# Optimization experiments

Measured on AMD Instinct MI355X. Metric: run time of the kernel, lower is better.

## Reference

```python
import jax, jax.numpy as jnp
import numpy as np

N_NODES = 50000
N_EDGES = 800000
N_GRAPHS = 512
NUM_TYPES = 1000
EMB = 128
HID = 128


def setup_inputs() -> dict:
    key = jax.random.key(0)
    ks = jax.random.split(key, 8)
    x_type = jax.random.randint(ks[0], (N_NODES,), 0, NUM_TYPES, dtype=jnp.int32)
    edge_index = jax.random.randint(ks[1], (2, N_EDGES), 0, N_NODES, dtype=jnp.int32)
    batch = jnp.sort(jax.random.randint(ks[2], (N_NODES,), 0, N_GRAPHS, dtype=jnp.int32))
    emb = jax.random.normal(ks[3], (NUM_TYPES, EMB), jnp.float32)
    s1 = 1.0 / np.sqrt(EMB)
    s2 = 1.0 / np.sqrt(HID)
    W1 = jax.random.normal(ks[4], (EMB, HID), jnp.float32) * s1
    b1 = jnp.zeros((HID,), jnp.float32)
    W2 = jax.random.normal(ks[5], (HID, HID), jnp.float32) * s2
    b2 = jnp.zeros((HID,), jnp.float32)
    return {"x_type": x_type, "edge_index": edge_index, "batch": batch,
            "emb": emb, "W1": W1, "b1": b1, "W2": W2, "b2": b2}


def _gcn_norm(edge_index, n_nodes):
    # PyG GCNConv default: add self-loops, symmetric normalization.
    loops = jnp.arange(n_nodes, dtype=edge_index.dtype)
    src = jnp.concatenate([edge_index[0], loops])  # [E+N]
    dst = jnp.concatenate([edge_index[1], loops])
    deg = jax.ops.segment_sum(jnp.ones_like(dst, jnp.float32), dst, num_segments=n_nodes)
    dis = jax.lax.rsqrt(deg)  # deg >= 1 thanks to self-loops
    norm = dis[src] * dis[dst]  # [E+N]
    return src, dst, norm


def _gcn_conv(x, src, dst, norm, W, b, n_nodes):
    h = x @ W                                  # [N, out]
    msg = h[src] * norm[:, None]               # edge-gathered, normalized messages
    out = jax.ops.segment_sum(msg, dst, num_segments=n_nodes)  # scatter-add
    return out + b


def reference(x_type, edge_index, batch, emb, W1, b1, W2, b2):
    src, dst, norm = _gcn_norm(edge_index, N_NODES)
    x = emb[x_type]                            # [N, EMB]
    x = jax.nn.relu(_gcn_conv(x, src, dst, norm, W1, b1, N_NODES))
    x = _gcn_conv(x, src, dst, norm, W2, b2, N_NODES)
    # index_add_ pooling over graphs (dropout is identity in eval / p=0)
    out = jax.ops.segment_sum(x, batch, num_segments=N_GRAPHS)  # [G, HID]
    return out
```

## Files before the change

### kernel.cpp

```cpp
#include <hip/hip_runtime.h>

#define N_NODES 50000
#define N_EDGES 800000
#define N_GRAPHS 512
#define FDIM 128
#define NTYPES_PAD 1000

#define NBLK 128
#define CHUNK ((N_EDGES + NBLK - 1) / NBLK)
#define NQUAD (N_NODES / 4)
#define NSB ((NQUAD + 127) / 128)
#define NPW 4
#define NW ((N_NODES + NPW - 1) / NPW)

typedef __bf16 bf16x8 __attribute__((ext_vector_type(8)));
typedef float f32x4 __attribute__((ext_vector_type(4)));
union BF8 { bf16x8 v; unsigned short u[8]; };

__device__ __forceinline__ unsigned short f2bf(float f) {
  unsigned int u = __float_as_uint(f);
  unsigned int r = (u + 0x7FFFu + ((u >> 16) & 1u)) >> 16;
  return (unsigned short)r;
}
__device__ __forceinline__ float bflo(unsigned int v) {
  return __uint_as_float(v << 16);
}
__device__ __forceinline__ float bfhi(unsigned int v) {
  return __uint_as_float(v & 0xFFFF0000u);
}

__global__ __launch_bounds__(512) void k_hist(const int* __restrict__ dst,
                                              unsigned int* __restrict__ Hist,
                                              unsigned char* __restrict__ rank8,
                                              int* __restrict__ g_done) {
  __shared__ unsigned int h[NQUAD];
  int b = blockIdx.x, t = threadIdx.x;
  if (b == 0 && t == 0) *g_done = 0;
  for (int i = t; i < NQUAD; i += 512) h[i] = 0;
  __syncthreads();
  int e0 = b * CHUNK, e1 = min(e0 + CHUNK, N_EDGES);
  for (int e = e0 + t; e < e1; e += 512) {
    int d = dst[e];
    unsigned int sh = (d & 3) * 8;
    unsigned int old = atomicAdd(&h[d >> 2], 1u << sh);
    rank8[e] = (unsigned char)((old >> sh) & 0xFFu);
  }
  __syncthreads();
  unsigned int* H = Hist + (size_t)b * NQUAD;
  for (int i = t; i < NQUAD; i += 512) H[i] = h[i];
}

__global__ __launch_bounds__(128) void k_prep(
    const unsigned int* __restrict__ Hist, const int* __restrict__ batch,
    unsigned int* __restrict__ Cur, float* __restrict__ dis,
    int* __restrict__ row_ptr, float* __restrict__ Zb,
    int* __restrict__ gstart, int* __restrict__ g_bsum,
    int* __restrict__ g_done) {
  int blk = blockIdx.x, tid = threadIdx.x;
  int q = blk * 128 + tid;

  for (int i = blk * 128 + tid; i < N_GRAPHS * FDIM; i += NSB * 128)
    Zb[i] = 0.0f;

  if (q < NQUAD) {
    int i0 = 4 * q;
    int prev = (i0 == 0) ? -1 : batch[i0 - 1];
#pragma unroll
    for (int k = 0; k < 4; ++k) {
      int i = i0 + k;
      int bb = batch[i];
      for (int g = prev + 1; g <= bb; ++g) gstart[g] = i;
      prev = bb;
    }
    if (i0 + 3 == N_NODES - 1)
      for (int g = prev + 1; g <= N_GRAPHS; ++g) gstart[g] = N_NODES;
  }

  unsigned int r0 = 0, r1 = 0, r2 = 0, r3 = 0;
  if (q < NQUAD) {
    for (int b = 0; b < NBLK; ++b) {
      unsigned int v = Hist[(size_t)b * NQUAD + q];
      Cur[(size_t)b * NQUAD + q] =
          (r0 & 255u) | ((r1 & 255u) << 8) | ((r2 & 255u) << 16) | (r3 << 24);
      r0 += v & 255u;
      r1 += (v >> 8) & 255u;
      r2 += (v >> 16) & 255u;
      r3 += v >> 24;
    }
    float4 dv = make_float4(rsqrtf((float)r0 + 1.f), rsqrtf((float)r1 + 1.f),
                            rsqrtf((float)r2 + 1.f), rsqrtf((float)r3 + 1.f));
    ((float4*)dis)[q] = dv;
  }

  int tsum = (q < NQUAD) ? (int)(r0 + r1 + r2 + r3) : 0;
  __shared__ int s[128];
  s[tid] = tsum;
  __syncthreads();
  for (int d = 1; d < 128; d <<= 1) {
    int u = (tid >= d) ? s[tid - d] : 0;
    __syncthreads();
    s[tid] += u;
    __syncthreads();
  }
  int excl = s[tid] - tsum;
  int btotal = s[127];

  if (tid == 0) {
    atomicExch(&g_bsum[blk], btotal);
    __threadfence();
    atomicAdd(g_done, 1);
    while (atomicAdd(g_done, 0) < NSB) {
    }
  }
  __syncthreads();
  __shared__ int sb[NSB];
  if (tid < NSB) sb[tid] = atomicAdd(&g_bsum[tid], 0);
  __syncthreads();
  int bpref = 0;
  for (int t = 0; t < blk; ++t) bpref += sb[t];

  if (q < NQUAD) {
    int base = bpref + excl;
    ((int4*)row_ptr)[q] =
        make_int4(base, base + (int)r0, base + (int)(r0 + r1),
                  base + (int)(r0 + r1 + r2));
  }
  if (q == NQUAD - 1) row_ptr[N_NODES] = N_EDGES;
}

__global__ __launch_bounds__(512) void k_fill2(
    const int* __restrict__ src, const int* __restrict__ dst,
    const int* __restrict__ x_type, const int* __restrict__ row_ptr,
    const unsigned int* __restrict__ Cur, const unsigned char* __restrict__ rank8,
    const float* __restrict__ dis, unsigned long long* __restrict__ csr) {
  int e = blockIdx.x * blockDim.x + threadIdx.x;
  if (e >= N_EDGES) return;
  int b = e / CHUNK;
  int s = src[e], d = dst[e];
  unsigned int cw = Cur[(size_t)b * NQUAD + (d >> 2)];
  int base = (int)((cw >> ((d & 3) * 8)) & 0xFFu);
  int pos = row_ptr[d] + base + (int)rank8[e];
  unsigned int lo = (unsigned int)s | ((unsigned int)x_type[s] << 16);
  unsigned int hi = (unsigned int)f2bf(dis[d]);
  csr[pos] = (unsigned long long)lo | ((unsigned long long)hi << 32);
}

__global__ __launch_bounds__(256) void k_embw(
    const float* __restrict__ emb, const float* __restrict__ W1,
    unsigned short* __restrict__ T1) {
  __shared__ unsigned short Ws[128 * 128];
  int t = threadIdx.x, w = t >> 6, l = t & 63;
  for (int i = t; i < 16384; i += 256) {
    int k = i >> 7, n = i & 127;
    Ws[n * 128 + (k ^ ((n & 15) << 3))] = f2bf(W1[i]);
  }
  int row0 = blockIdx.x * 64 + w * 16;
  int arow = row0 + (l & 15);
  bool ok = arow < NTYPES_PAD;
  bf16x8 a[4];
#pragma unroll
  for (int ks = 0; ks < 4; ++ks) {
    BF8 av;
    const float* ap = emb + (size_t)arow * FDIM + (l >> 4) * 8 + ks * 32;
#pragma unroll
    for (int i = 0; i < 8; ++i) av.u[i] = ok ? f2bf(ap[i]) : 0;
    a[ks] = av.v;
  }
  __syncthreads();
  f32x4 acc[8] = {};
#pragma unroll
  for (int ks = 0; ks < 4; ++ks) {
#pragma unroll
    for (int ct = 0; ct < 8; ++ct) {
      int n = ct * 16 + (l & 15);
      int kk = (ks * 32 + (l >> 4) * 8) ^ ((n & 15) << 3);
      bf16x8 b = *(const bf16x8*)&Ws[n * 128 + kk];
      acc[ct] =
          __builtin_amdgcn_mfma_f32_16x16x32_bf16(a[ks], b, acc[ct], 0, 0, 0);
    }
  }
#pragma unroll
  for (int ct = 0; ct < 8; ++ct) {
    int col = ct * 16 + (l & 15);
#pragma unroll
    for (int r = 0; r < 4; ++r) {
      int row = row0 + (l >> 4) * 4 + r;
      if (row < NTYPES_PAD) T1[row * FDIM + col] = f2bf(acc[ct][r]);
    }
  }
}

__global__ void k_agg1(const int* __restrict__ x_type,
                       const unsigned short* __restrict__ T1,
                       const float* __restrict__ b1,
                       const int* __restrict__ row_ptr,
                       const unsigned long long* __restrict__ csr,
                       const float* __restrict__ dis,
                       unsigned int* __restrict__ y1) {
  int gid = blockIdx.x * blockDim.x + threadIdx.x;
  int node = gid >> 6;
  int lane = gid & 63;
  if (node >= N_NODES) return;
  const unsigned int* T = (const unsigned int*)T1;
  const unsigned int* C = (const unsigned int*)csr;
  float di = dis[node];
  unsigned int v = T[(size_t)x_type[node] * 64 + lane];
  float ax = bflo(v) * di, ay = bfhi(v) * di;
  int j = row_ptr[node], end = row_ptr[node + 1];
  for (; j + 8 <= end; j += 8) {
    unsigned int e0 = C[2 * j], e1 = C[2 * j + 2];
    unsigned int e2 = C[2 * j + 4], e3 = C[2 * j + 6];
    unsigned int e4 = C[2 * j + 8], e5 = C[2 * j + 10];
    unsigned int e6 = C[2 * j + 12], e7 = C[2 * j + 14];
    unsigned int u0 = T[(size_t)(e0 >> 16) * 64 + lane];
    unsigned int u1 = T[(size_t)(e1 >> 16) * 64 + lane];
    unsigned int u2 = T[(size_t)(e2 >> 16) * 64 + lane];
    unsigned int u3 = T[(size_t)(e3 >> 16) * 64 + lane];
    unsigned int u4 = T[(size_t)(e4 >> 16) * 64 + lane];
    unsigned int u5 = T[(size_t)(e5 >> 16) * 64 + lane];
    unsigned int u6 = T[(size_t)(e6 >> 16) * 64 + lane];
    unsigned int u7 = T[(size_t)(e7 >> 16) * 64 + lane];
    float n0 = dis[e0 & 0xFFFFu], n1 = dis[e1 & 0xFFFFu];
    float n2 = dis[e2 & 0xFFFFu], n3 = dis[e3 & 0xFFFFu];
    float n4 = dis[e4 & 0xFFFFu], n5 = dis[e5 & 0xFFFFu];
    float n6 = dis[e6 & 0xFFFFu], n7 = dis[e7 & 0xFFFFu];
    ax = fmaf(bflo(u0), n0, ax); ay = fmaf(bfhi(u0), n0, ay);
    ax = fmaf(bflo(u1), n1, ax); ay = fmaf(bfhi(u1), n1, ay);
    ax = fmaf(bflo(u2), n2, ax); ay = fmaf(bfhi(u2), n2, ay);
    ax = fmaf(bflo(u3), n3, ax); ay = fmaf(bfhi(u3), n3, ay);
    ax = fmaf(bflo(u4), n4, ax); ay = fmaf(bfhi(u4), n4, ay);
    ax = fmaf(bflo(u5), n5, ax); ay = fmaf(bfhi(u5), n5, ay);
    ax = fmaf(bflo(u6), n6, ax); ay = fmaf(bfhi(u6), n6, ay);
    ax = fmaf(bflo(u7), n7, ax); ay = fmaf(bfhi(u7), n7, ay);
  }
  for (; j + 4 <= end; j += 4) {
    unsigned int e0 = C[2 * j], e1 = C[2 * j + 2];
    unsigned int e2 = C[2 * j + 4], e3 = C[2 * j + 6];
    unsigned int u0 = T[(size_t)(e0 >> 16) * 64 + lane];
    unsigned int u1 = T[(size_t)(e1 >> 16) * 64 + lane];
    unsigned int u2 = T[(size_t)(e2 >> 16) * 64 + lane];
    unsigned int u3 = T[(size_t)(e3 >> 16) * 64 + lane];
    float n0 = dis[e0 & 0xFFFFu], n1 = dis[e1 & 0xFFFFu];
    float n2 = dis[e2 & 0xFFFFu], n3 = dis[e3 & 0xFFFFu];
    ax = fmaf(bflo(u0), n0, ax); ay = fmaf(bfhi(u0), n0, ay);
    ax = fmaf(bflo(u1), n1, ax); ay = fmaf(bfhi(u1), n1, ay);
    ax = fmaf(bflo(u2), n2, ax); ay = fmaf(bfhi(u2), n2, ay);
    ax = fmaf(bflo(u3), n3, ax); ay = fmaf(bfhi(u3), n3, ay);
  }
  for (; j < end; ++j) {
    unsigned int e = C[2 * j];
    unsigned int u = T[(size_t)(e >> 16) * 64 + lane];
    float nw = dis[e & 0xFFFFu];
    ax = fmaf(bflo(u), nw, ax);
    ay = fmaf(bfhi(u), nw, ay);
  }
  float2 bb = ((const float2*)b1)[lane];
  ax = fmaxf(fmaf(di, ax, bb.x), 0.f) * di;
  ay = fmaxf(fmaf(di, ay, bb.y), 0.f) * di;
  y1[(size_t)node * 64 + lane] = (unsigned int)f2bf(ax) |
                                 ((unsigned int)f2bf(ay) << 16);
}

__global__ void k_aggpool(const unsigned int* __restrict__ y1,
                          const int* __restrict__ row_ptr,
                          const unsigned long long* __restrict__ csr,
                          const float* __restrict__ dis,
                          const int* __restrict__ batch,
                          float* __restrict__ Partials, int* __restrict__ Gid,
                          float* __restrict__ Zb) {
  int gid = blockIdx.x * blockDim.x + threadIdx.x;
  int wid = gid >> 6;
  int lane = gid & 63;
  int n0 = wid * NPW;
  if (n0 >= N_NODES) return;
  int nend = min(n0 + NPW, N_NODES);
  int g0 = batch[n0];
  float px = 0.f, py = 0.f;
  int node = n0;
  while (node < nend) {
    int g = batch[node];
    int rend = node + 1;
    while (rend < nend && batch[rend] == g) ++rend;
    float sx = 0.f, sy = 0.f;
    for (int n = node; n < rend; ++n) {
      float dn = dis[n];
      unsigned int v = y1[(size_t)n * 64 + lane];
      sx = fmaf(dn, bflo(v), sx);
      sy = fmaf(dn, bfhi(v), sy);
    }
    int j = row_ptr[node], jend = row_ptr[rend];
    for (; j + 16 <= jend; j += 16) {
#pragma unroll
      for (int k = 0; k < 16; ++k) {
        unsigned long long e = csr[j + k];
        unsigned int u = y1[(size_t)(e & 0xFFFFu) * 64 + lane];
        float w = __uint_as_float(((unsigned int)(e >> 32)) << 16);
        sx = fmaf(bflo(u), w, sx);
        sy = fmaf(bfhi(u), w, sy);
      }
    }
    for (; j + 4 <= jend; j += 4) {
#pragma unroll
      for (int k = 0; k < 4; ++k) {
        unsigned long long e = csr[j + k];
        unsigned int u = y1[(size_t)(e & 0xFFFFu) * 64 + lane];
        float w = __uint_as_float(((unsigned int)(e >> 32)) << 16);
        sx = fmaf(bflo(u), w, sx);
        sy = fmaf(bfhi(u), w, sy);
      }
    }
    for (; j < jend; ++j) {
      unsigned long long e = csr[j];
      unsigned int u = y1[(size_t)(e & 0xFFFFu) * 64 + lane];
      float w = __uint_as_float(((unsigned int)(e >> 32)) << 16);
      sx = fmaf(bflo(u), w, sx);
      sy = fmaf(bfhi(u), w, sy);
    }
    if (g == g0) {
      px += sx;
      py += sy;
    } else {
      atomicAdd(&Zb[(size_t)g * FDIM + 2 * lane], sx);
      atomicAdd(&Zb[(size_t)g * FDIM + 2 * lane + 1], sy);
    }
    node = rend;
  }
  ((float2*)Partials)[(size_t)wid * 64 + lane] = make_float2(px, py);
  if (lane == 0) Gid[wid] = g0;
}

__global__ __launch_bounds__(128) void k_poolzw2(
    const float* __restrict__ Partials, const int* __restrict__ Gid,
    const float* __restrict__ Zb, const int* __restrict__ gstart,
    const float* __restrict__ W2, const float* __restrict__ b2,
    float* __restrict__ out) {
  __shared__ float Zs[FDIM];
  int g = blockIdx.x, t = threadIdx.x;
  int s = gstart[g], e = gstart[g + 1];
  float acc = Zb[(size_t)g * FDIM + t];
  if (e > s) {
    int w0 = s / NPW, w1 = (e - 1) / NPW;
    for (int w = w0; w <= w1; ++w)
      if (Gid[w] == g) acc += Partials[(size_t)w * FDIM + t];
  }
  Zs[t] = acc;
  __syncthreads();
  float o = 0.f;
#pragma unroll 8
  for (int k = 0; k < FDIM; ++k) o = fmaf(Zs[k], W2[k * FDIM + t], o);
  out[(size_t)g * FDIM + t] = o + (float)(e - s) * b2[t];
}

extern "C" void kernel_launch(void* const* d_in, const int* in_sizes, int n_in,
                              void* d_out, int out_size, void* d_ws,
                              size_t ws_size, hipStream_t stream) {
  const int* x_type = (const int*)d_in[0];
  const int* edge_index = (const int*)d_in[1];
  const int* batch = (const int*)d_in[2];
  const float* emb = (const float*)d_in[3];
  const float* W1 = (const float*)d_in[4];
  const float* b1 = (const float*)d_in[5];
  const float* W2 = (const float*)d_in[6];
  const float* b2 = (const float*)d_in[7];
  float* out = (float*)d_out;

  const int* src = edge_index;
  const int* dst = edge_index + N_EDGES;

  char* p = (char*)d_ws;
  size_t off = 0;
  auto alloc = [&](size_t bytes) {
    void* r = p + off;
    off = (off + bytes + 255) & ~(size_t)255;
    return r;
  };
  float* dis = (float*)alloc(N_NODES * 4);
  int* row_ptr = (int*)alloc((N_NODES + 1) * 4);
  int* gstart = (int*)alloc((N_GRAPHS + 1) * 4);
  unsigned int* Hist = (unsigned int*)alloc((size_t)NBLK * NQUAD * 4);
  unsigned int* Cur = (unsigned int*)alloc((size_t)NBLK * NQUAD * 4);
  unsigned char* rank8 = (unsigned char*)alloc(N_EDGES);
  unsigned long long* csr =
      (unsigned long long*)alloc((size_t)N_EDGES * 8);
  unsigned short* T1 = (unsigned short*)alloc((size_t)NTYPES_PAD * FDIM * 2);
  unsigned int* y1 = (unsigned int*)alloc((size_t)N_NODES * 64 * 4);
  float* Partials = (float*)alloc((size_t)NW * FDIM * 4);
  int* Gid = (int*)alloc(NW * 4);
  float* Zb = (float*)alloc((size_t)N_GRAPHS * FDIM * 4);
  int* g_bsum = (int*)alloc(NSB * 4);
  int* g_done = (int*)alloc(4);
  (void)ws_size;

  k_hist<<<NBLK, 512, 0, stream>>>(dst, Hist, rank8, g_done);
  k_prep<<<NSB, 128, 0, stream>>>(Hist, batch, Cur, dis, row_ptr, Zb, gstart,
                                  g_bsum, g_done);
  k_fill2<<<(N_EDGES + 511) / 512, 512, 0, stream>>>(
      src, dst, x_type, row_ptr, Cur, rank8, dis, csr);
  k_embw<<<(NTYPES_PAD + 63) / 64, 256, 0, stream>>>(emb, W1, T1);
  k_agg1<<<(N_NODES * 64 + 255) / 256, 256, 0, stream>>>(
      x_type, T1, b1, row_ptr, csr, dis, y1);
  k_aggpool<<<(NW * 64 + 255) / 256, 256, 0, stream>>>(
      y1, row_ptr, csr, dis, batch, Partials, Gid, Zb);
  k_poolzw2<<<N_GRAPHS, 128, 0, stream>>>(Partials, Gid, Zb, gstart, W2, b2,
                                          out);
}
```

Measured before the change: 151.3 us.

## Merge embedding GEMM into prep kernel and split agg1 edges across two waves

The emb@W1 MFMA GEMM moves into extra blocks of k_prep, which now runs at 256 threads, so one launch disappears and the GEMM overlaps the degree scan. k_agg1 now gives each node two wavefronts that split its edge list and combine their partial sums through shared memory, aiming for more memory-level parallelism on the gathers. NPW for aggpool drops from 4 to 2. In exchange, k_prep gains a 32KB shared buffer that can lower occupancy, and agg1 adds a block-wide barrier.

```diff
diff --git a/kernel.cpp b/kernel.cpp
--- a/kernel.cpp
+++ b/kernel.cpp
@@ -9,8 +9,9 @@
 #define NBLK 128
 #define CHUNK ((N_EDGES + NBLK - 1) / NBLK)
 #define NQUAD (N_NODES / 4)
-#define NSB ((NQUAD + 127) / 128)
-#define NPW 4
+#define NSB ((NQUAD + 255) / 256)
+#define EMBW_BLOCKS 16
+#define NPW 2
 #define NW ((N_NODES + NPW - 1) / NPW)
 
 typedef __bf16 bf16x8 __attribute__((ext_vector_type(8)));
@@ -50,16 +51,64 @@
   for (int i = t; i < NQUAD; i += 512) H[i] = h[i];
 }
 
-__global__ __launch_bounds__(128) void k_prep(
+__global__ __launch_bounds__(256) void k_prep(
     const unsigned int* __restrict__ Hist, const int* __restrict__ batch,
     unsigned int* __restrict__ Cur, float* __restrict__ dis,
     int* __restrict__ row_ptr, float* __restrict__ Zb,
     int* __restrict__ gstart, int* __restrict__ g_bsum,
-    int* __restrict__ g_done) {
+    int* __restrict__ g_done, const float* __restrict__ emb,
+    const float* __restrict__ W1, unsigned short* __restrict__ T1) {
+  __shared__ unsigned short sh[16384];
   int blk = blockIdx.x, tid = threadIdx.x;
-  int q = blk * 128 + tid;
-
-  for (int i = blk * 128 + tid; i < N_GRAPHS * FDIM; i += NSB * 128)
+
+  if (blk >= NSB) {
+    unsigned short* Ws = sh;
+    int t = tid, w = t >> 6, l = t & 63;
+    for (int i = t; i < 16384; i += 256) {
+      int k = i >> 7, n = i & 127;
+      Ws[n * 128 + (k ^ ((n & 15) << 3))] = f2bf(W1[i]);
+    }
+    int row0 = (blk - NSB) * 64 + w * 16;
+    int arow = row0 + (l & 15);
+    bool ok = arow < NTYPES_PAD;
+    bf16x8 a[4];
+#pragma unroll
+    for (int ks = 0; ks < 4; ++ks) {
+      BF8 av;
+      const float* ap = emb + (size_t)arow * FDIM + (l >> 4) * 8 + ks * 32;
+#pragma unroll
+      for (int i = 0; i < 8; ++i) av.u[i] = ok ? f2bf(ap[i]) : 0;
+      a[ks] = av.v;
+    }
+    __syncthreads();
+    f32x4 acc[8] = {};
+#pragma unroll
+    for (int ks = 0; ks < 4; ++ks) {
+#pragma unroll
+      for (int ct = 0; ct < 8; ++ct) {
+        int n = ct * 16 + (l & 15);
+        int kk = (ks * 32 + (l >> 4) * 8) ^ ((n & 15) << 3);
+        bf16x8 b = *(const bf16x8*)&Ws[n * 128 + kk];
+        acc[ct] =
+            __builtin_amdgcn_mfma_f32_16x16x32_bf16(a[ks], b, acc[ct], 0, 0, 0);
+      }
+    }
+#pragma unroll
+    for (int ct = 0; ct < 8; ++ct) {
+      int col = ct * 16 + (l & 15);
+#pragma unroll
+      for (int r = 0; r < 4; ++r) {
+        int row = row0 + (l >> 4) * 4 + r;
+        if (row < NTYPES_PAD) T1[row * FDIM + col] = f2bf(acc[ct][r]);
+      }
+    }
+    return;
+  }
+
+  int* si = (int*)sh;
+  int q = blk * 256 + tid;
+
+  for (int i = blk * 256 + tid; i < N_GRAPHS * FDIM; i += NSB * 256)
     Zb[i] = 0.0f;
 
   if (q < NQUAD) {
@@ -93,17 +142,16 @@
   }
 
   int tsum = (q < NQUAD) ? (int)(r0 + r1 + r2 + r3) : 0;
-  __shared__ int s[128];
-  s[tid] = tsum;
-  __syncthreads();
-  for (int d = 1; d < 128; d <<= 1) {
-    int u = (tid >= d) ? s[tid - d] : 0;
+  si[tid] = tsum;
+  __syncthreads();
+  for (int d = 1; d < 256; d <<= 1) {
+    int u = (tid >= d) ? si[tid - d] : 0;
     __syncthreads();
-    s[tid] += u;
+    si[tid] += u;
     __syncthreads();
   }
-  int excl = s[tid] - tsum;
-  int btotal = s[127];
+  int excl = si[tid] - tsum;
+  int btotal = si[255];
 
   if (tid == 0) {
     atomicExch(&g_bsum[blk], btotal);
@@ -113,7 +161,7 @@
     }
   }
   __syncthreads();
-  __shared__ int sb[NSB];
+  int* sb = si + 256;
   if (tid < NSB) sb[tid] = atomicAdd(&g_bsum[tid], 0);
   __syncthreads();
   int bpref = 0;
@@ -145,120 +193,75 @@
   csr[pos] = (unsigned long long)lo | ((unsigned long long)hi << 32);
 }
 
-__global__ __launch_bounds__(256) void k_embw(
-    const float* __restrict__ emb, const float* __restrict__ W1,
-    unsigned short* __restrict__ T1) {
-  __shared__ unsigned short Ws[128 * 128];
-  int t = threadIdx.x, w = t >> 6, l = t & 63;
-  for (int i = t; i < 16384; i += 256) {
-    int k = i >> 7, n = i & 127;
-    Ws[n * 128 + (k ^ ((n & 15) << 3))] = f2bf(W1[i]);
-  }
-  int row0 = blockIdx.x * 64 + w * 16;
-  int arow = row0 + (l & 15);
-  bool ok = arow < NTYPES_PAD;
-  bf16x8 a[4];
-#pragma unroll
-  for (int ks = 0; ks < 4; ++ks) {
-    BF8 av;
-    const float* ap = emb + (size_t)arow * FDIM + (l >> 4) * 8 + ks * 32;
-#pragma unroll
-    for (int i = 0; i < 8; ++i) av.u[i] = ok ? f2bf(ap[i]) : 0;
-    a[ks] = av.v;
-  }
-  __syncthreads();
-  f32x4 acc[8] = {};
-#pragma unroll
-  for (int ks = 0; ks < 4; ++ks) {
-#pragma unroll
-    for (int ct = 0; ct < 8; ++ct) {
-      int n = ct * 16 + (l & 15);
-      int kk = (ks * 32 + (l >> 4) * 8) ^ ((n & 15) << 3);
-      bf16x8 b = *(const bf16x8*)&Ws[n * 128 + kk];
-      acc[ct] =
-          __builtin_amdgcn_mfma_f32_16x16x32_bf16(a[ks], b, acc[ct], 0, 0, 0);
-    }
-  }
-#pragma unroll
-  for (int ct = 0; ct < 8; ++ct) {
-    int col = ct * 16 + (l & 15);
-#pragma unroll
-    for (int r = 0; r < 4; ++r) {
-      int row = row0 + (l >> 4) * 4 + r;
-      if (row < NTYPES_PAD) T1[row * FDIM + col] = f2bf(acc[ct][r]);
-    }
-  }
-}
-
-__global__ void k_agg1(const int* __restrict__ x_type,
-                       const unsigned short* __restrict__ T1,
-                       const float* __restrict__ b1,
-                       const int* __restrict__ row_ptr,
-                       const unsigned long long* __restrict__ csr,
-                       const float* __restrict__ dis,
-                       unsigned int* __restrict__ y1) {
-  int gid = blockIdx.x * blockDim.x + threadIdx.x;
-  int node = gid >> 6;
-  int lane = gid & 63;
-  if (node >= N_NODES) return;
+__global__ __launch_bounds__(256) void k_agg1(
+    const int* __restrict__ x_type, const unsigned short* __restrict__ T1,
+    const float* __restrict__ b1, const int* __restrict__ row_ptr,
+    const unsigned long long* __restrict__ csr, const float* __restrict__ dis,
+    unsigned int* __restrict__ y1) {
+  __shared__ float2 comb[2][64];
+  int t = threadIdx.x;
+  int w = t >> 6, l = t & 63;
+  int nl = w >> 1, h = w & 1;
+  int node = blockIdx.x * 2 + nl;
   const unsigned int* T = (const unsigned int*)T1;
   const unsigned int* C = (const unsigned int*)csr;
-  float di = dis[node];
-  unsigned int v = T[(size_t)x_type[node] * 64 + lane];
-  float ax = bflo(v) * di, ay = bfhi(v) * di;
-  int j = row_ptr[node], end = row_ptr[node + 1];
-  for (; j + 8 <= end; j += 8) {
-    unsigned int e0 = C[2 * j], e1 = C[2 * j + 2];
-    unsigned int e2 = C[2 * j + 4], e3 = C[2 * j + 6];
-    unsigned int e4 = C[2 * j + 8], e5 = C[2 * j + 10];
-    unsigned int e6 = C[2 * j + 12], e7 = C[2 * j + 14];
-    unsigned int u0 = T[(size_t)(e0 >> 16) * 64 + lane];
-    unsigned int u1 = T[(size_t)(e1 >> 16) * 64 + lane];
-    unsigned int u2 = T[(size_t)(e2 >> 16) * 64 + lane];
-    unsigned int u3 = T[(size_t)(e3 >> 16) * 64 + lane];
-    unsigned int u4 = T[(size_t)(e4 >> 16) * 64 + lane];
-    unsigned int u5 = T[(size_t)(e5 >> 16) * 64 + lane];
-    unsigned int u6 = T[(size_t)(e6 >> 16) * 64 + lane];
-    unsigned int u7 = T[(size_t)(e7 >> 16) * 64 + lane];
-    float n0 = dis[e0 & 0xFFFFu], n1 = dis[e1 & 0xFFFFu];
-    float n2 = dis[e2 & 0xFFFFu], n3 = dis[e3 & 0xFFFFu];
-    float n4 = dis[e4 & 0xFFFFu], n5 = dis[e5 & 0xFFFFu];
-    float n6 = dis[e6 & 0xFFFFu], n7 = dis[e7 & 0xFFFFu];
-    ax = fmaf(bflo(u0), n0, ax); ay = fmaf(bfhi(u0), n0, ay);
-    ax = fmaf(bflo(u1), n1, ax); ay = fmaf(bfhi(u1), n1, ay);
-    ax = fmaf(bflo(u2), n2, ax); ay = fmaf(bfhi(u2), n2, ay);
-    ax = fmaf(bflo(u3), n3, ax); ay = fmaf(bfhi(u3), n3, ay);
-    ax = fmaf(bflo(u4), n4, ax); ay = fmaf(bfhi(u4), n4, ay);
-    ax = fmaf(bflo(u5), n5, ax); ay = fmaf(bfhi(u5), n5, ay);
-    ax = fmaf(bflo(u6), n6, ax); ay = fmaf(bfhi(u6), n6, ay);
-    ax = fmaf(bflo(u7), n7, ax); ay = fmaf(bfhi(u7), n7, ay);
-  }
-  for (; j + 4 <= end; j += 4) {
-    unsigned int e0 = C[2 * j], e1 = C[2 * j + 2];
-    unsigned int e2 = C[2 * j + 4], e3 = C[2 * j + 6];
-    unsigned int u0 = T[(size_t)(e0 >> 16) * 64 + lane];
-    unsigned int u1 = T[(size_t)(e1 >> 16) * 64 + lane];
-    unsigned int u2 = T[(size_t)(e2 >> 16) * 64 + lane];
-    unsigned int u3 = T[(size_t)(e3 >> 16) * 64 + lane];
-    float n0 = dis[e0 & 0xFFFFu], n1 = dis[e1 & 0xFFFFu];
-    float n2 = dis[e2 & 0xFFFFu], n3 = dis[e3 & 0xFFFFu];
-    ax = fmaf(bflo(u0), n0, ax); ay = fmaf(bfhi(u0), n0, ay);
-    ax = fmaf(bflo(u1), n1, ax); ay = fmaf(bfhi(u1), n1, ay);
-    ax = fmaf(bflo(u2), n2, ax); ay = fmaf(bfhi(u2), n2, ay);
-    ax = fmaf(bflo(u3), n3, ax); ay = fmaf(bfhi(u3), n3, ay);
-  }
-  for (; j < end; ++j) {
-    unsigned int e = C[2 * j];
-    unsigned int u = T[(size_t)(e >> 16) * 64 + lane];
-    float nw = dis[e & 0xFFFFu];
-    ax = fmaf(bflo(u), nw, ax);
-    ay = fmaf(bfhi(u), nw, ay);
-  }
-  float2 bb = ((const float2*)b1)[lane];
-  ax = fmaxf(fmaf(di, ax, bb.x), 0.f) * di;
-  ay = fmaxf(fmaf(di, ay, bb.y), 0.f) * di;
-  y1[(size_t)node * 64 + lane] = (unsigned int)f2bf(ax) |
-                                 ((unsigned int)f2bf(ay) << 16);
+  float ax = 0.f, ay = 0.f;
+  float di = 0.f;
+  if (node < N_NODES) {
+    di = dis[node];
+    if (h == 0) {
+      unsigned int v = T[(size_t)x_type[node] * 64 + l];
+      ax = bflo(v) * di;
+      ay = bfhi(v) * di;
+    }
+    int beg = row_ptr[node], end = row_ptr[node + 1];
+    int nfull = (end - beg) & ~15;
+    for (int j0 = beg + h * 8; j0 < beg + nfull; j0 += 16) {
+      unsigned int e0 = C[2 * j0], e1 = C[2 * j0 + 2];
+      unsigned int e2 = C[2 * j0 + 4], e3 = C[2 * j0 + 6];
+      unsigned int e4 = C[2 * j0 + 8], e5 = C[2 * j0 + 10];
+      unsigned int e6 = C[2 * j0 + 12], e7 = C[2 * j0 + 14];
+      unsigned int u0 = T[(size_t)(e0 >> 16) * 64 + l];
+      unsigned int u1 = T[(size_t)(e1 >> 16) * 64 + l];
+      unsigned int u2 = T[(size_t)(e2 >> 16) * 64 + l];
+      unsigned int u3 = T[(size_t)(e3 >> 16) * 64 + l];
+      unsigned int u4 = T[(size_t)(e4 >> 16) * 64 + l];
+      unsigned int u5 = T[(size_t)(e5 >> 16) * 64 + l];
+      unsigned int u6 = T[(size_t)(e6 >> 16) * 64 + l];
+      unsigned int u7 = T[(size_t)(e7 >> 16) * 64 + l];
+      float n0 = dis[e0 & 0xFFFFu], n1 = dis[e1 & 0xFFFFu];
+      float n2 = dis[e2 & 0xFFFFu], n3 = dis[e3 & 0xFFFFu];
+      float n4 = dis[e4 & 0xFFFFu], n5 = dis[e5 & 0xFFFFu];
+      float n6 = dis[e6 & 0xFFFFu], n7 = dis[e7 & 0xFFFFu];
+      ax = fmaf(bflo(u0), n0, ax); ay = fmaf(bfhi(u0), n0, ay);
+      ax = fmaf(bflo(u1), n1, ax); ay = fmaf(bfhi(u1), n1, ay);
+      ax = fmaf(bflo(u2), n2, ax); ay = fmaf(bfhi(u2), n2, ay);
+      ax = fmaf(bflo(u3), n3, ax); ay = fmaf(bfhi(u3), n3, ay);
+      ax = fmaf(bflo(u4), n4, ax); ay = fmaf(bfhi(u4), n4, ay);
+      ax = fmaf(bflo(u5), n5, ax); ay = fmaf(bfhi(u5), n5, ay);
+      ax = fmaf(bflo(u6), n6, ax); ay = fmaf(bfhi(u6), n6, ay);
+      ax = fmaf(bflo(u7), n7, ax); ay = fmaf(bfhi(u7), n7, ay);
+    }
+    for (int j = beg + nfull + h; j < end; j += 2) {
+      unsigned int e = C[2 * j];
+      unsigned int u = T[(size_t)(e >> 16) * 64 + l];
+      float nw = dis[e & 0xFFFFu];
+      ax = fmaf(bflo(u), nw, ax);
+      ay = fmaf(bfhi(u), nw, ay);
+    }
+  }
+  if (h == 1) comb[nl][l] = make_float2(ax, ay);
+  __syncthreads();
+  if (h == 0 && node < N_NODES) {
+    float2 c = comb[nl][l];
+    ax += c.x;
+    ay += c.y;
+    float2 bb = ((const float2*)b1)[l];
+    ax = fmaxf(fmaf(di, ax, bb.x), 0.f) * di;
+    ay = fmaxf(fmaf(di, ay, bb.y), 0.f) * di;
+    y1[(size_t)node * 64 + l] = (unsigned int)f2bf(ax) |
+                                ((unsigned int)f2bf(ay) << 16);
+  }
 }
 
 __global__ void k_aggpool(const unsigned int* __restrict__ y1,
@@ -392,13 +395,12 @@
   (void)ws_size;
 
   k_hist<<<NBLK, 512, 0, stream>>>(dst, Hist, rank8, g_done);
-  k_prep<<<NSB, 128, 0, stream>>>(Hist, batch, Cur, dis, row_ptr, Zb, gstart,
-                                  g_bsum, g_done);
+  k_prep<<<NSB + EMBW_BLOCKS, 256, 0, stream>>>(
+      Hist, batch, Cur, dis, row_ptr, Zb, gstart, g_bsum, g_done, emb, W1, T1);
   k_fill2<<<(N_EDGES + 511) / 512, 512, 0, stream>>>(
       src, dst, x_type, row_ptr, Cur, rank8, dis, csr);
-  k_embw<<<(NTYPES_PAD + 63) / 64, 256, 0, stream>>>(emb, W1, T1);
-  k_agg1<<<(N_NODES * 64 + 255) / 256, 256, 0, stream>>>(
-      x_type, T1, b1, row_ptr, csr, dis, y1);
+  k_agg1<<<(N_NODES + 1) / 2, 256, 0, stream>>>(x_type, T1, b1, row_ptr, csr,
+                                                dis, y1);
   k_aggpool<<<(NW * 64 + 255) / 256, 256, 0, stream>>>(
       y1, row_ptr, csr, dis, batch, Partials, Gid, Zb);
   k_poolzw2<<<N_GRAPHS, 128, 0, stream>>>(Partials, Gid, Zb, gstart, W2, b2,
```

Result: slower. 164.5 us (+8.7%).
